# Optimization experiments

Measured on AMD Instinct MI355X. Metric: run time of the kernel, lower is better.

Reference implementation:

```python
import jax, jax.numpy as jnp
import numpy as np

N, C, D = 131072, 512, 3


def setup_inputs() -> dict:
    key = jax.random.key(0)
    kx, kmu = jax.random.split(key)
    X = jax.random.normal(kx, (N, D), dtype=jnp.float32)
    mu = jax.random.normal(kmu, (C, D), dtype=jnp.float32)
    w = jnp.zeros((C,), dtype=jnp.float32)
    # sigma as in __init__: r = sqrt(sum of per-dim unbiased variances of mu0)
    r = jnp.sqrt(jnp.var(mu, axis=0, ddof=1).sum())
    sigma = (0.1 * (r / C ** (1.0 / D))).astype(jnp.float32)
    return {"X": X, "mu": mu, "w": w, "sigma": sigma}


def reference(X, mu, w, sigma):
    # One EM step of a uniform-covariance GMM (EM_step_pytorch).
    n, d = X.shape
    # pairwise squared distances [N, C]
    D2_nc = ((X[:, None, :] - mu[None, :, :]) ** 2).sum(-1)
    # log-responsibilities (E-step), softmax over components
    lgamma_nc = jax.nn.log_softmax(w[None, :] - D2_nc / (2.0 * sigma ** 2), axis=1)
    gamma_nc = jnp.exp(lgamma_nc)
    # M-step: centroids (softmax over points, per component)
    mu_new = jax.nn.softmax(lgamma_nc, axis=0).T @ X  # [C, D]
    # M-step: component scores
    h_c = jax.nn.logsumexp(lgamma_nc, axis=0)  # [C]
    w_new = h_c - h_c.mean()
    # M-step: uniform std
    sigma_new = jnp.sqrt((gamma_nc * D2_nc).sum() / (d * n))
    # EM values: expected targets and free energy
    Y = gamma_nc @ mu_new  # [N, D]
    logpi_c = w_new - jax.nn.logsumexp(w_new)
    Cfe = (gamma_nc * (
        ((mu_new ** 2).sum(-1)[None, :] - (Y ** 2).sum(-1)[:, None]) / (2.0 * sigma_new ** 2)
        + d * jnp.log(sigma_new)
        - logpi_c[None, :]
        + lgamma_nc
    )).sum()
    return Y, Cfe
```

## Files before the change

### kernel.cpp

```cpp
#include <hip/hip_runtime.h>
#include <cfloat>
#include <cmath>

#define NPTS 131072
#define NC   512

#define PM4_OFF  0
#define PQ4_OFF  2048
#define S_OFF    4096
#define T_OFF    4608
#define MISC_OFF 6144

__device__ __forceinline__ float waveSum(float v) {
#pragma unroll
  for (int off = 32; off > 0; off >>= 1) v += __shfl_down(v, off, 64);
  return v;
}
__device__ __forceinline__ float waveMax(float v) {
#pragma unroll
  for (int off = 32; off > 0; off >>= 1) v = fmaxf(v, __shfl_down(v, off, 64));
  return v;
}

__global__ __launch_bounds__(512) void k_prep(
    const float* __restrict__ mu, const float* __restrict__ w,
    const float* __restrict__ sigma, float4* __restrict__ pm,
    float* __restrict__ Sacc, float* __restrict__ Tacc,
    float* __restrict__ misc) {
  const int t = threadIdx.x;
  const float sg = sigma[0];
  const float inv2s2 = 1.0f / (2.0f * sg * sg);
  const float m0 = mu[3 * t], m1 = mu[3 * t + 1], m2 = mu[3 * t + 2];
  pm[t] = make_float4(2.0f * inv2s2 * m0, 2.0f * inv2s2 * m1, 2.0f * inv2s2 * m2,
                      w[t] - (m0 * m0 + m1 * m1 + m2 * m2) * inv2s2);
  Sacc[t] = 0.f;
  Tacc[3 * t] = 0.f;
  Tacc[3 * t + 1] = 0.f;
  Tacc[3 * t + 2] = 0.f;
  if (t < 8) misc[t] = 0.f;
}

__global__ __launch_bounds__(1024, 4) void k_estep(
    const float* __restrict__ X, const float4* __restrict__ pm,
    float* __restrict__ Sacc, float* __restrict__ Tacc,
    float* __restrict__ misc, float* __restrict__ out) {
  __shared__ float4 s_pt[256];
  __shared__ float2 s_ms[4][256];
  __shared__ float4 s_half[512];
  __shared__ float  s_red[16];

  const int t = threadIdx.x;
  const int p = t & 255;
  const int ch = __builtin_amdgcn_readfirstlane(t >> 8);
  const int n = blockIdx.x * 256 + p;
  const float x0 = X[3 * n], x1 = X[3 * n + 1], x2 = X[3 * n + 2];

  const float4* __restrict__ pmc = pm + ch * 128;
  float ma = -FLT_MAX, mb = -FLT_MAX;
#pragma unroll 8
  for (int i = 0; i < 128; i += 2) {
    float4 a = pmc[i], b = pmc[i + 1];
    ma = fmaxf(ma, fmaf(a.x, x0, fmaf(a.y, x1, fmaf(a.z, x2, a.w))));
    mb = fmaxf(mb, fmaf(b.x, x0, fmaf(b.y, x1, fmaf(b.z, x2, b.w))));
  }
  const float m = fmaxf(ma, mb);
  float sa = 0.f, sb = 0.f;
#pragma unroll 8
  for (int i = 0; i < 128; i += 2) {
    float4 a = pmc[i], b = pmc[i + 1];
    sa += __expf(fmaf(a.x, x0, fmaf(a.y, x1, fmaf(a.z, x2, a.w))) - m);
    sb += __expf(fmaf(b.x, x0, fmaf(b.y, x1, fmaf(b.z, x2, b.w))) - m);
  }
  s_ms[ch][p] = make_float2(m, sa + sb);
  __syncthreads();

  if (ch == 0) {
    float2 q0 = s_ms[0][p], q1 = s_ms[1][p], q2 = s_ms[2][p], q3 = s_ms[3][p];
    float M = fmaxf(fmaxf(q0.x, q1.x), fmaxf(q2.x, q3.x));
    float SS = q0.y * __expf(q0.x - M) + q1.y * __expf(q1.x - M) +
               q2.y * __expf(q2.x - M) + q3.y * __expf(q3.x - M);
    float z = M + __logf(SS);
    s_pt[p] = make_float4(x0, x1, x2, z);
    out[3 * n] = z;
  }
  __syncthreads();

  const int comp = t & 511;
  const int half = __builtin_amdgcn_readfirstlane(t >> 9);
  const float4 pc = pm[comp];
  const float4* sp = s_pt + half * 128;
  float Sg = 0.f, Tx = 0.f, Ty = 0.f, Tz = 0.f;
#pragma unroll 4
  for (int i = 0; i < 128; ++i) {
    float4 pt = sp[i];
    float l = fmaf(pc.x, pt.x, fmaf(pc.y, pt.y, fmaf(pc.z, pt.z, pc.w)));
    float g = __expf(l - pt.w);
    Sg += g;
    Tx = fmaf(g, pt.x, Tx);
    Ty = fmaf(g, pt.y, Ty);
    Tz = fmaf(g, pt.z, Tz);
  }
  if (half) s_half[comp] = make_float4(Tx, Ty, Tz, Sg);
  __syncthreads();
  if (!half) {
    float4 o = s_half[comp];
    atomicAdd(&Sacc[comp], Sg + o.w);
    atomicAdd(&Tacc[3 * comp], Tx + o.x);
    atomicAdd(&Tacc[3 * comp + 1], Ty + o.y);
    atomicAdd(&Tacc[3 * comp + 2], Tz + o.z);
  }

  float q = (ch == 0) ? (x0 * x0 + x1 * x1 + x2 * x2) : 0.f;
  float r = waveSum(q);
  if ((t & 63) == 0) s_red[t >> 6] = r;
  __syncthreads();
  if (t == 0) {
    float v = 0.f;
#pragma unroll
    for (int i = 0; i < 16; ++i) v += s_red[i];
    atomicAdd(&misc[0], v);
  }
}

__global__ __launch_bounds__(512) void k_mstep(
    const float* __restrict__ mu, const float* __restrict__ Sacc,
    const float* __restrict__ Tacc, float4* __restrict__ pq,
    float* __restrict__ misc, float* __restrict__ out) {
  __shared__ float s_red[8];
  __shared__ float s_red2[8];
  __shared__ float s_bc[4];
  const int t = threadIdx.x;

  const float S = Sacc[t];
  const float Sc = fmaxf(S, 1e-30f);
  const float h = __logf(Sc);
  const float T0 = Tacc[3 * t], T1 = Tacc[3 * t + 1], T2 = Tacc[3 * t + 2];
  const float m0 = T0 / Sc, m1 = T1 / Sc, m2 = T2 / Sc;

  const float o0 = mu[3 * t], o1 = mu[3 * t + 1], o2 = mu[3 * t + 2];
  const float gdp = S * (o0 * o0 + o1 * o1 + o2 * o2)
                    - 2.0f * (o0 * T0 + o1 * T1 + o2 * T2);

  float hm = waveMax(h);
  if ((t & 63) == 0) s_red[t >> 6] = hm;
  __syncthreads();
  if (t == 0) {
    float v = s_red[0];
    for (int i = 1; i < 8; ++i) v = fmaxf(v, s_red[i]);
    s_bc[0] = v;
  }
  __syncthreads();
  const float hM = s_bc[0];

  float es = waveSum(__expf(h - hM));
  float gs = waveSum(gdp);
  if ((t & 63) == 0) { s_red[t >> 6] = es; s_red2[t >> 6] = gs; }
  __syncthreads();
  if (t == 0) {
    float esum = 0.f, gsum = 0.f;
    for (int i = 0; i < 8; ++i) { esum += s_red[i]; gsum += s_red2[i]; }
    s_bc[1] = hM + __logf(esum);
    const float gd = fmaxf(misc[0] + gsum, 1e-20f);
    const float sn2 = gd * (1.0f / (3.0f * (float)NPTS));
    s_bc[2] = 1.0f / (2.0f * sn2);
    s_bc[3] = 1.5f * __logf(sn2);
  }
  __syncthreads();

  const float logpi = h - s_bc[1];
  const float A = (m0 * m0 + m1 * m1 + m2 * m2) * s_bc[2] - logpi;
  pq[t] = make_float4(m0, m1, m2, A);
  if (t == 0) {
    misc[1] = s_bc[2];
    misc[2] = s_bc[3];
    out[NPTS * 3] = 0.f;
  }
}

__global__ __launch_bounds__(1024, 4) void k_final(
    const float* __restrict__ X, const float4* __restrict__ pm,
    const float4* __restrict__ pq, const float* __restrict__ misc,
    float* __restrict__ out) {
  __shared__ float4 s_y[4][256];
  __shared__ float  s_g[4][256];
  __shared__ float  s_red[16];

  const int t = threadIdx.x;
  const int p = t & 255;
  const int ch = __builtin_amdgcn_readfirstlane(t >> 8);
  const int n = blockIdx.x * 256 + p;
  const float x0 = X[3 * n], x1 = X[3 * n + 1], x2 = X[3 * n + 2];
  const float z = out[3 * n];
  const float inv2s2n = misc[1], dlogsig = misc[2];

  const float4* __restrict__ pmc = pm + ch * 128;
  const float4* __restrict__ pqc = pq + ch * 128;
  float y0 = 0.f, y1 = 0.f, y2 = 0.f, acc = 0.f, sg = 0.f;
#pragma unroll 4
  for (int i = 0; i < 128; ++i) {
    float4 pp = pmc[i];
    float4 qq = pqc[i];
    float l = fmaf(pp.x, x0, fmaf(pp.y, x1, fmaf(pp.z, x2, pp.w))) - z;
    float g = __expf(l);
    sg += g;
    y0 = fmaf(g, qq.x, y0);
    y1 = fmaf(g, qq.y, y1);
    y2 = fmaf(g, qq.z, y2);
    acc = fmaf(g, qq.w + l, acc);
  }
  s_y[ch][p] = make_float4(y0, y1, y2, acc);
  s_g[ch][p] = sg;
  __syncthreads();

  float cfe = 0.f;
  if (ch == 0) {
    float4 a0 = s_y[0][p], a1 = s_y[1][p], a2 = s_y[2][p], a3 = s_y[3][p];
    float Y0 = a0.x + a1.x + a2.x + a3.x;
    float Y1 = a0.y + a1.y + a2.y + a3.y;
    float Y2 = a0.z + a1.z + a2.z + a3.z;
    float A  = a0.w + a1.w + a2.w + a3.w;
    float G  = s_g[0][p] + s_g[1][p] + s_g[2][p] + s_g[3][p];
    float yn2 = Y0 * Y0 + Y1 * Y1 + Y2 * Y2;
    cfe = A + G * (dlogsig - yn2 * inv2s2n);
    out[3 * n] = Y0;
    out[3 * n + 1] = Y1;
    out[3 * n + 2] = Y2;
  }
  float r = waveSum(cfe);
  if ((t & 63) == 0) s_red[t >> 6] = r;
  __syncthreads();
  if (t == 0) {
    float v = 0.f;
#pragma unroll
    for (int i = 0; i < 16; ++i) v += s_red[i];
    atomicAdd(&out[NPTS * 3], v);
  }
}

extern "C" void kernel_launch(void* const* d_in, const int* in_sizes, int n_in,
                              void* d_out, int out_size, void* d_ws, size_t ws_size,
                              hipStream_t stream) {
  const float* X = (const float*)d_in[0];
  const float* mu = (const float*)d_in[1];
  const float* w = (const float*)d_in[2];
  const float* sigma = (const float*)d_in[3];
  float* out = (float*)d_out;
  float* ws = (float*)d_ws;

  float4* pm = (float4*)(ws + PM4_OFF);
  float4* pq = (float4*)(ws + PQ4_OFF);
  float* Sacc = ws + S_OFF;
  float* Tacc = ws + T_OFF;
  float* misc = ws + MISC_OFF;

  k_prep<<<1, 512, 0, stream>>>(mu, w, sigma, pm, Sacc, Tacc, misc);
  k_estep<<<NPTS / 256, 1024, 0, stream>>>(X, pm, Sacc, Tacc, misc, out);
  k_mstep<<<1, 512, 0, stream>>>(mu, Sacc, Tacc, pq, misc, out);
  k_final<<<NPTS / 256, 1024, 0, stream>>>(X, pm, pq, misc, out);
}
```

Before: 163.1 us.

## Move free-energy terms into E/M steps and replicate atomic accumulators

Rewrites the free-energy sum so the per-point gamma*(A+l) and gamma*dlogsig terms become per-component S*A plus a global sum of gamma*lgamma computed in the E-step. This removes those accumulators from the final pass. Component statistics are now accumulated into NREP interleaved float4 replicas to cut atomic contention, and mstep sums the replicas. Both big kernels shrink to 512-thread blocks of 128 points, which doubles the number of blocks and the atomic traffic per point. The reassociated sums may change float rounding slightly.

Result: faster. 146.0 us (-10.5%).

```diff
diff --git a/kernel.cpp b/kernel.cpp
--- a/kernel.cpp
+++ b/kernel.cpp
@@ -4,12 +4,12 @@
 
 #define NPTS 131072
 #define NC   512
+#define NREP 4
 
 #define PM4_OFF  0
 #define PQ4_OFF  2048
-#define S_OFF    4096
-#define T_OFF    4608
-#define MISC_OFF 6144
+#define ST4_OFF  4096
+#define MISC_OFF 12288
 
 __device__ __forceinline__ float waveSum(float v) {
 #pragma unroll
@@ -25,121 +25,123 @@
 __global__ __launch_bounds__(512) void k_prep(
     const float* __restrict__ mu, const float* __restrict__ w,
     const float* __restrict__ sigma, float4* __restrict__ pm,
-    float* __restrict__ Sacc, float* __restrict__ Tacc,
-    float* __restrict__ misc) {
+    float* __restrict__ ST, float* __restrict__ misc) {
   const int t = threadIdx.x;
   const float sg = sigma[0];
   const float inv2s2 = 1.0f / (2.0f * sg * sg);
   const float m0 = mu[3 * t], m1 = mu[3 * t + 1], m2 = mu[3 * t + 2];
   pm[t] = make_float4(2.0f * inv2s2 * m0, 2.0f * inv2s2 * m1, 2.0f * inv2s2 * m2,
                       w[t] - (m0 * m0 + m1 * m1 + m2 * m2) * inv2s2);
-  Sacc[t] = 0.f;
-  Tacc[3 * t] = 0.f;
-  Tacc[3 * t + 1] = 0.f;
-  Tacc[3 * t + 2] = 0.f;
+#pragma unroll
+  for (int r = 0; r < NREP * 4; ++r) ST[r * 512 + t] = 0.f;
   if (t < 8) misc[t] = 0.f;
 }
 
-__global__ __launch_bounds__(1024, 4) void k_estep(
+__global__ __launch_bounds__(512, 8) void k_estep(
     const float* __restrict__ X, const float4* __restrict__ pm,
-    float* __restrict__ Sacc, float* __restrict__ Tacc,
-    float* __restrict__ misc, float* __restrict__ out) {
-  __shared__ float4 s_pt[256];
-  __shared__ float2 s_ms[4][256];
-  __shared__ float4 s_half[512];
-  __shared__ float  s_red[16];
-
-  const int t = threadIdx.x;
-  const int p = t & 255;
-  const int ch = __builtin_amdgcn_readfirstlane(t >> 8);
-  const int n = blockIdx.x * 256 + p;
+    float* __restrict__ ST, float* __restrict__ misc,
+    float* __restrict__ out) {
+  __shared__ float4 s_pt[128];
+  __shared__ float2 s_ms[4][128];
+  __shared__ float  s_red[8];
+  __shared__ float  s_red2[8];
+
+  const int t = threadIdx.x;
+  const int p = t & 127;
+  const int ch = __builtin_amdgcn_readfirstlane(t >> 7);
+  const int n = blockIdx.x * 128 + p;
   const float x0 = X[3 * n], x1 = X[3 * n + 1], x2 = X[3 * n + 2];
 
   const float4* __restrict__ pmc = pm + ch * 128;
-  float ma = -FLT_MAX, mb = -FLT_MAX;
-#pragma unroll 8
-  for (int i = 0; i < 128; i += 2) {
-    float4 a = pmc[i], b = pmc[i + 1];
+  float ma = -FLT_MAX, mb = -FLT_MAX, mc = -FLT_MAX, md = -FLT_MAX;
+#pragma unroll 4
+  for (int i = 0; i < 128; i += 4) {
+    float4 a = pmc[i], b = pmc[i + 1], c = pmc[i + 2], d = pmc[i + 3];
     ma = fmaxf(ma, fmaf(a.x, x0, fmaf(a.y, x1, fmaf(a.z, x2, a.w))));
     mb = fmaxf(mb, fmaf(b.x, x0, fmaf(b.y, x1, fmaf(b.z, x2, b.w))));
-  }
-  const float m = fmaxf(ma, mb);
-  float sa = 0.f, sb = 0.f;
-#pragma unroll 8
-  for (int i = 0; i < 128; i += 2) {
-    float4 a = pmc[i], b = pmc[i + 1];
+    mc = fmaxf(mc, fmaf(c.x, x0, fmaf(c.y, x1, fmaf(c.z, x2, c.w))));
+    md = fmaxf(md, fmaf(d.x, x0, fmaf(d.y, x1, fmaf(d.z, x2, d.w))));
+  }
+  const float m = fmaxf(fmaxf(ma, mb), fmaxf(mc, md));
+  float sa = 0.f, sb = 0.f, sc = 0.f, sd = 0.f;
+#pragma unroll 4
+  for (int i = 0; i < 128; i += 4) {
+    float4 a = pmc[i], b = pmc[i + 1], c = pmc[i + 2], d = pmc[i + 3];
     sa += __expf(fmaf(a.x, x0, fmaf(a.y, x1, fmaf(a.z, x2, a.w))) - m);
     sb += __expf(fmaf(b.x, x0, fmaf(b.y, x1, fmaf(b.z, x2, b.w))) - m);
-  }
-  s_ms[ch][p] = make_float2(m, sa + sb);
-  __syncthreads();
-
-  if (ch == 0) {
-    float2 q0 = s_ms[0][p], q1 = s_ms[1][p], q2 = s_ms[2][p], q3 = s_ms[3][p];
+    sc += __expf(fmaf(c.x, x0, fmaf(c.y, x1, fmaf(c.z, x2, c.w))) - m);
+    sd += __expf(fmaf(d.x, x0, fmaf(d.y, x1, fmaf(d.z, x2, d.w))) - m);
+  }
+  s_ms[ch][p] = make_float2(m, (sa + sb) + (sc + sd));
+  __syncthreads();
+
+  if (t < 128) {
+    float2 q0 = s_ms[0][t], q1 = s_ms[1][t], q2 = s_ms[2][t], q3 = s_ms[3][t];
     float M = fmaxf(fmaxf(q0.x, q1.x), fmaxf(q2.x, q3.x));
     float SS = q0.y * __expf(q0.x - M) + q1.y * __expf(q1.x - M) +
                q2.y * __expf(q2.x - M) + q3.y * __expf(q3.x - M);
     float z = M + __logf(SS);
-    s_pt[p] = make_float4(x0, x1, x2, z);
+    s_pt[t] = make_float4(x0, x1, x2, z);
     out[3 * n] = z;
   }
   __syncthreads();
 
-  const int comp = t & 511;
-  const int half = __builtin_amdgcn_readfirstlane(t >> 9);
-  const float4 pc = pm[comp];
-  const float4* sp = s_pt + half * 128;
-  float Sg = 0.f, Tx = 0.f, Ty = 0.f, Tz = 0.f;
+  const float4 pc = pm[t];
+  float Sg = 0.f, Tx = 0.f, Ty = 0.f, Tz = 0.f, La = 0.f;
 #pragma unroll 4
   for (int i = 0; i < 128; ++i) {
-    float4 pt = sp[i];
+    float4 pt = s_pt[i];
     float l = fmaf(pc.x, pt.x, fmaf(pc.y, pt.y, fmaf(pc.z, pt.z, pc.w)));
-    float g = __expf(l - pt.w);
+    float d = l - pt.w;
+    float g = __expf(d);
     Sg += g;
     Tx = fmaf(g, pt.x, Tx);
     Ty = fmaf(g, pt.y, Ty);
     Tz = fmaf(g, pt.z, Tz);
-  }
-  if (half) s_half[comp] = make_float4(Tx, Ty, Tz, Sg);
-  __syncthreads();
-  if (!half) {
-    float4 o = s_half[comp];
-    atomicAdd(&Sacc[comp], Sg + o.w);
-    atomicAdd(&Tacc[3 * comp], Tx + o.x);
-    atomicAdd(&Tacc[3 * comp + 1], Ty + o.y);
-    atomicAdd(&Tacc[3 * comp + 2], Tz + o.z);
-  }
-
-  float q = (ch == 0) ? (x0 * x0 + x1 * x1 + x2 * x2) : 0.f;
-  float r = waveSum(q);
-  if ((t & 63) == 0) s_red[t >> 6] = r;
-  __syncthreads();
-  if (t == 0) {
-    float v = 0.f;
-#pragma unroll
-    for (int i = 0; i < 16; ++i) v += s_red[i];
-    atomicAdd(&misc[0], v);
+    La = fmaf(g, d, La);
+  }
+  float* st = ST + (((blockIdx.x & (NREP - 1)) * 512 + t) << 2);
+  atomicAdd(st + 0, Tx);
+  atomicAdd(st + 1, Ty);
+  atomicAdd(st + 2, Tz);
+  atomicAdd(st + 3, Sg);
+
+  float xx = (t < 128) ? (x0 * x0 + x1 * x1 + x2 * x2) : 0.f;
+  float rx = waveSum(xx);
+  float rl = waveSum(La);
+  if ((t & 63) == 0) { s_red[t >> 6] = rx; s_red2[t >> 6] = rl; }
+  __syncthreads();
+  if (t == 0) {
+    float vx = 0.f, vl = 0.f;
+#pragma unroll
+    for (int i = 0; i < 8; ++i) { vx += s_red[i]; vl += s_red2[i]; }
+    atomicAdd(&misc[0], vx);
+    atomicAdd(&misc[3], vl);
   }
 }
 
 __global__ __launch_bounds__(512) void k_mstep(
-    const float* __restrict__ mu, const float* __restrict__ Sacc,
-    const float* __restrict__ Tacc, float4* __restrict__ pq,
-    float* __restrict__ misc, float* __restrict__ out) {
+    const float* __restrict__ mu, const float4* __restrict__ ST4,
+    float4* __restrict__ pq, float* __restrict__ misc,
+    float* __restrict__ out) {
   __shared__ float s_red[8];
   __shared__ float s_red2[8];
   __shared__ float s_bc[4];
   const int t = threadIdx.x;
 
-  const float S = Sacc[t];
+  float Tx = 0.f, Ty = 0.f, Tz = 0.f, S = 0.f;
+#pragma unroll
+  for (int r = 0; r < NREP; ++r) {
+    float4 v = ST4[r * 512 + t];
+    Tx += v.x; Ty += v.y; Tz += v.z; S += v.w;
+  }
   const float Sc = fmaxf(S, 1e-30f);
   const float h = __logf(Sc);
-  const float T0 = Tacc[3 * t], T1 = Tacc[3 * t + 1], T2 = Tacc[3 * t + 2];
-  const float m0 = T0 / Sc, m1 = T1 / Sc, m2 = T2 / Sc;
+  const float m0 = Tx / Sc, m1 = Ty / Sc, m2 = Tz / Sc;
 
   const float o0 = mu[3 * t], o1 = mu[3 * t + 1], o2 = mu[3 * t + 2];
   const float gdp = S * (o0 * o0 + o1 * o1 + o2 * o2)
-                    - 2.0f * (o0 * T0 + o1 * T1 + o2 * T2);
+                    - 2.0f * (o0 * Tx + o1 * Ty + o2 * Tz);
 
   float hm = waveMax(h);
   if ((t & 63) == 0) s_red[t >> 6] = hm;
@@ -167,61 +169,60 @@
   }
   __syncthreads();
 
+  const float inv2s2n = s_bc[2];
   const float logpi = h - s_bc[1];
-  const float A = (m0 * m0 + m1 * m1 + m2 * m2) * s_bc[2] - logpi;
+  const float A = (m0 * m0 + m1 * m1 + m2 * m2) * inv2s2n - logpi;
   pq[t] = make_float4(m0, m1, m2, A);
-  if (t == 0) {
-    misc[1] = s_bc[2];
-    misc[2] = s_bc[3];
-    out[NPTS * 3] = 0.f;
-  }
-}
-
-__global__ __launch_bounds__(1024, 4) void k_final(
+
+  float ca = waveSum(S * A);
+  if ((t & 63) == 0) s_red[t >> 6] = ca;
+  __syncthreads();
+  if (t == 0) {
+    float v = 0.f;
+    for (int i = 0; i < 8; ++i) v += s_red[i];
+    out[NPTS * 3] = v + misc[3] + (float)NPTS * s_bc[3];
+    misc[1] = inv2s2n;
+  }
+}
+
+__global__ __launch_bounds__(512, 8) void k_final(
     const float* __restrict__ X, const float4* __restrict__ pm,
     const float4* __restrict__ pq, const float* __restrict__ misc,
     float* __restrict__ out) {
-  __shared__ float4 s_y[4][256];
-  __shared__ float  s_g[4][256];
-  __shared__ float  s_red[16];
-
-  const int t = threadIdx.x;
-  const int p = t & 255;
-  const int ch = __builtin_amdgcn_readfirstlane(t >> 8);
-  const int n = blockIdx.x * 256 + p;
+  __shared__ float4 s_y[4][128];
+  __shared__ float  s_red[8];
+
+  const int t = threadIdx.x;
+  const int p = t & 127;
+  const int ch = __builtin_amdgcn_readfirstlane(t >> 7);
+  const int n = blockIdx.x * 128 + p;
   const float x0 = X[3 * n], x1 = X[3 * n + 1], x2 = X[3 * n + 2];
   const float z = out[3 * n];
-  const float inv2s2n = misc[1], dlogsig = misc[2];
+  const float inv2s2n = misc[1];
 
   const float4* __restrict__ pmc = pm + ch * 128;
   const float4* __restrict__ pqc = pq + ch * 128;
-  float y0 = 0.f, y1 = 0.f, y2 = 0.f, acc = 0.f, sg = 0.f;
+  float y0 = 0.f, y1 = 0.f, y2 = 0.f;
 #pragma unroll 4
   for (int i = 0; i < 128; ++i) {
     float4 pp = pmc[i];
     float4 qq = pqc[i];
     float l = fmaf(pp.x, x0, fmaf(pp.y, x1, fmaf(pp.z, x2, pp.w))) - z;
     float g = __expf(l);
-    sg += g;
     y0 = fmaf(g, qq.x, y0);
     y1 = fmaf(g, qq.y, y1);
     y2 = fmaf(g, qq.z, y2);
-    acc = fmaf(g, qq.w + l, acc);
-  }
-  s_y[ch][p] = make_float4(y0, y1, y2, acc);
-  s_g[ch][p] = sg;
+  }
+  s_y[ch][p] = make_float4(y0, y1, y2, 0.f);
   __syncthreads();
 
   float cfe = 0.f;
-  if (ch == 0) {
-    float4 a0 = s_y[0][p], a1 = s_y[1][p], a2 = s_y[2][p], a3 = s_y[3][p];
-    float Y0 = a0.x + a1.x + a2.x + a3.x;
-    float Y1 = a0.y + a1.y + a2.y + a3.y;
-    float Y2 = a0.z + a1.z + a2.z + a3.z;
-    float A  = a0.w + a1.w + a2.w + a3.w;
-    float G  = s_g[0][p] + s_g[1][p] + s_g[2][p] + s_g[3][p];
-    float yn2 = Y0 * Y0 + Y1 * Y1 + Y2 * Y2;
-    cfe = A + G * (dlogsig - yn2 * inv2s2n);
+  if (t < 128) {
+    float4 a0 = s_y[0][t], a1 = s_y[1][t], a2 = s_y[2][t], a3 = s_y[3][t];
+    float Y0 = (a0.x + a1.x) + (a2.x + a3.x);
+    float Y1 = (a0.y + a1.y) + (a2.y + a3.y);
+    float Y2 = (a0.z + a1.z) + (a2.z + a3.z);
+    cfe = -(Y0 * Y0 + Y1 * Y1 + Y2 * Y2) * inv2s2n;
     out[3 * n] = Y0;
     out[3 * n + 1] = Y1;
     out[3 * n + 2] = Y2;
@@ -232,7 +233,7 @@
   if (t == 0) {
     float v = 0.f;
 #pragma unroll
-    for (int i = 0; i < 16; ++i) v += s_red[i];
+    for (int i = 0; i < 8; ++i) v += s_red[i];
     atomicAdd(&out[NPTS * 3], v);
   }
 }
@@ -249,12 +250,11 @@
 
   float4* pm = (float4*)(ws + PM4_OFF);
   float4* pq = (float4*)(ws + PQ4_OFF);
-  float* Sacc = ws + S_OFF;
-  float* Tacc = ws + T_OFF;
+  float* ST = ws + ST4_OFF;
   float* misc = ws + MISC_OFF;
 
-  k_prep<<<1, 512, 0, stream>>>(mu, w, sigma, pm, Sacc, Tacc, misc);
-  k_estep<<<NPTS / 256, 1024, 0, stream>>>(X, pm, Sacc, Tacc, misc, out);
-  k_mstep<<<1, 512, 0, stream>>>(mu, Sacc, Tacc, pq, misc, out);
-  k_final<<<NPTS / 256, 1024, 0, stream>>>(X, pm, pq, misc, out);
-}
+  k_prep<<<1, 512, 0, stream>>>(mu, w, sigma, pm, ST, misc);
+  k_estep<<<NPTS / 128, 512, 0, stream>>>(X, pm, ST, misc, out);
+  k_mstep<<<1, 512, 0, stream>>>(mu, (const float4*)ST, pq, misc, out);
+  k_final<<<NPTS / 128, 512, 0, stream>>>(X, pm, pq, misc, out);
+}
```
